# Performance work log

Hardware: AMD Instinct MI355X
Metric: run time of the kernel (lower is better)

## Reference

```python
import jax, jax.numpy as jnp
import numpy as np

HIDDEN = 1024
B, S = 8, 2048

def setup_inputs() -> dict:
    key = jax.random.key(0)
    k1, k2, k3, k4 = jax.random.split(key, 4)
    gain = 1.2
    # xavier_uniform bound for square [H,H] weight
    bound = gain * np.sqrt(6.0 / (HIDDEN + HIDDEN))
    return {
        "hidden_states": jax.random.normal(k1, (B, S, HIDDEN), dtype=jnp.float32),
        "Wq": jax.random.uniform(k2, (HIDDEN, HIDDEN), jnp.float32, -bound, bound),
        "bq": jnp.zeros((HIDDEN,), jnp.float32),
        "Wv": jax.random.uniform(k3, (HIDDEN, HIDDEN), jnp.float32, -bound, bound),
        "bv": jnp.zeros((HIDDEN,), jnp.float32),
        "anomaly_matrix": jax.random.uniform(k4, (HIDDEN, HIDDEN), jnp.float32, -2.0, 2.0),
    }

def reference(hidden_states, Wq, bq, Wv, bv, anomaly_matrix):
    # input magnitude rescaling
    input_norm = jnp.linalg.norm(hidden_states, axis=-1, keepdims=True)  # [B,S,1]
    scaled = hidden_states / (input_norm + 1e-9)
    # torch nn.Linear: x @ W.T + b
    q = jnp.einsum('bsh,oh->bso', scaled, Wq) + bq  # [B,S,H]
    v = jnp.einsum('bsh,oh->bso', scaled, Wv) + bv  # [B,S,H]
    # bilinear anomaly score: q @ A, then q @ (qA)^T
    tq = jnp.einsum('bsh,hk->bsk', q, anomaly_matrix)  # [B,S,H]
    scores = jnp.einsum('bsh,bth->bst', q, tq) / jnp.sqrt(jnp.float32(HIDDEN))  # [B,S,S]
    probs = jax.nn.softmax(scores, axis=-1)
    # dropout is identity in eval mode
    ctx = jnp.einsum('bst,bth->bsh', probs, v)  # [B,S,H]
    return ctx * input_norm
```

## Files before the change

kernel.cpp:

```cpp
#include <hip/hip_runtime.h>
#include <cstdint>
#include <cstddef>

#define H 1024
#define BB 8
#define SS 2048
#define MROWS (BB*SS)

typedef float  f32x4 __attribute__((ext_vector_type(4)));
typedef short  s16x8 __attribute__((ext_vector_type(8)));
typedef unsigned short u16x4 __attribute__((ext_vector_type(4)));
typedef unsigned short u16x8 __attribute__((ext_vector_type(8)));

__device__ __forceinline__ float b2f(unsigned short u) {
  union { unsigned int i; float f; } x; x.i = ((unsigned int)u) << 16; return x.f;
}
__device__ __forceinline__ unsigned short f2b(float f) {
  union { float f; unsigned int i; } x; x.f = f;
  unsigned int r = x.i + 0x7FFFu + ((x.i >> 16) & 1u);
  return (unsigned short)(r >> 16);
}

typedef __attribute__((address_space(1))) unsigned int guint;
typedef __attribute__((address_space(3))) unsigned int luint;
__device__ __forceinline__ void gld_lds16(const void* g, void* l) {
  __builtin_amdgcn_global_load_lds((guint*)g, (luint*)l, 16, 0, 0);
}

__global__ void norms_cast(const float* __restrict__ X, unsigned short* __restrict__ Xs,
                           float* __restrict__ norms) {
  const int row  = blockIdx.x * 4 + (threadIdx.x >> 6);
  const int lane = threadIdx.x & 63;
  const float4* xr = (const float4*)(X + (size_t)row * H);
  float4 d[4]; float s = 0.f;
#pragma unroll
  for (int j = 0; j < 4; ++j) {
    d[j] = xr[lane + j * 64];
    s += d[j].x*d[j].x + d[j].y*d[j].y + d[j].z*d[j].z + d[j].w*d[j].w;
  }
#pragma unroll
  for (int o = 32; o; o >>= 1) s += __shfl_xor(s, o);
  const float nrm = sqrtf(s);
  const float inv = 1.f / (nrm + 1e-9f);
  if (lane == 0) norms[row] = nrm;
  unsigned short* xo = Xs + (size_t)row * H;
#pragma unroll
  for (int j = 0; j < 4; ++j) {
    u16x4 o4;
    o4[0] = f2b(d[j].x * inv); o4[1] = f2b(d[j].y * inv);
    o4[2] = f2b(d[j].z * inv); o4[3] = f2b(d[j].w * inv);
    *(u16x4*)(xo + (size_t)(lane + j * 64) * 4) = o4;
  }
}

__global__ void cast_f32_bf16(const float* __restrict__ in, unsigned short* __restrict__ out) {
  const size_t i = ((size_t)blockIdx.x * 256 + threadIdx.x) * 4;
  float4 d = *(const float4*)(in + i);
  u16x4 o; o[0] = f2b(d.x); o[1] = f2b(d.y); o[2] = f2b(d.z); o[3] = f2b(d.w);
  *(u16x4*)(out + i) = o;
}

__global__ void transpose_cast_f32(const float* __restrict__ in, unsigned short* __restrict__ out) {
  __shared__ float t[32][33];
  const int c0 = blockIdx.x * 32, r0 = blockIdx.y * 32;
  const int tx = threadIdx.x, ty = threadIdx.y;
#pragma unroll
  for (int j = 0; j < 4; ++j)
    t[ty + j * 8][tx] = in[(size_t)(r0 + ty + j * 8) * H + c0 + tx];
  __syncthreads();
#pragma unroll
  for (int j = 0; j < 4; ++j)
    out[(size_t)(c0 + ty + j * 8) * H + r0 + tx] = f2b(t[tx][ty + j * 8]);
}

__global__ void transpose_bf16(const unsigned short* __restrict__ in, unsigned short* __restrict__ out) {
  __shared__ unsigned short t[32][33];
  const size_t zo = (size_t)blockIdx.z * SS * H;
  const int c0 = blockIdx.x * 32, r0 = blockIdx.y * 32;
  const int tx = threadIdx.x, ty = threadIdx.y;
#pragma unroll
  for (int j = 0; j < 4; ++j)
    t[ty + j * 8][tx] = in[zo + (size_t)(r0 + ty + j * 8) * H + c0 + tx];
  __syncthreads();
#pragma unroll
  for (int j = 0; j < 4; ++j)
    out[zo + (size_t)(c0 + ty + j * 8) * SS + r0 + tx] = t[tx][ty + j * 8];
}

template <int EPI, int TK>
__global__ __launch_bounds__(512, 2)
void gemm_nt(const unsigned short* __restrict__ A, int lda,
             const unsigned short* __restrict__ B0, int ldb, long sB,
             void* __restrict__ Cv, int ldc,
             const float* __restrict__ bias,
             const float* __restrict__ norms, const float* __restrict__ rs) {
  __shared__ __align__(16) unsigned short lds[4][2][256 * 32];
  const int tid = threadIdx.x, lane = tid & 63, w = tid >> 6;

  const int nx = gridDim.x;
  int bid = blockIdx.y * nx + blockIdx.x;
  bid = (bid & 7) * ((nx * (int)gridDim.y) >> 3) + (bid >> 3);
  const int bn = bid % nx, bm = bid / nx;

  const unsigned short* Ap = A  + (size_t)bm * 256 * lda;
  const unsigned short* Bp = B0 + (size_t)(bm >> 3) * sB + (size_t)bn * 256 * ldb;

  const int sr    = tid >> 2;
  const int gslot = (tid & 3) ^ ((sr >> 1) & 3);
  const unsigned short* As0 = Ap + (size_t)sr * lda + gslot * 8;
  const unsigned short* Bs0 = Bp + (size_t)sr * ldb + gslot * 8;

  auto STAGE = [&](int kt, int q) {
    const unsigned short* as = As0 + kt * 32;
    const unsigned short* bs = Bs0 + kt * 32;
    unsigned short* la = &lds[q][0][0] + tid * 8;
    unsigned short* lb = &lds[q][1][0] + tid * 8;
    gld_lds16(as,                       la);
    gld_lds16(as + (size_t)128 * lda,   la + 4096);
    gld_lds16(bs,                       lb);
    gld_lds16(bs + (size_t)128 * ldb,   lb + 4096);
  };

  const int wm = w >> 2, wn = w & 3;
  const int rA = lane & 15;
  const int ssw = ((lane >> 4) ^ ((rA >> 1) & 3)) * 8;
  f32x4 acc[8][4] = {};

  auto COMPUTE = [&](int t) {
    const unsigned short* pa = &lds[t & 3][0][0] + (size_t)(wm * 128 + rA) * 32 + ssw;
    const unsigned short* pb = &lds[t & 3][1][0] + (size_t)(wn * 64  + rA) * 32 + ssw;
    s16x8 af[8], bf[4];
#pragma unroll
    for (int i = 0; i < 8; ++i) af[i] = *(const s16x8*)(pa + i * 512);
#pragma unroll
    for (int j = 0; j < 4; ++j) bf[j] = *(const s16x8*)(pb + j * 512);
    __builtin_amdgcn_s_setprio(1);
#pragma unroll
    for (int i = 0; i < 8; ++i)
#pragma unroll
      for (int j = 0; j < 4; ++j)
        acc[i][j] = __builtin_amdgcn_mfma_f32_16x16x32_bf16(af[i], bf[j], acc[i][j], 0, 0, 0);
    __builtin_amdgcn_s_setprio(0);
  };

  STAGE(0, 0);
  STAGE(1, 1);
#pragma unroll 1
  for (int t = 0; t < TK - 2; ++t) {
    STAGE(t + 2, (t + 2) & 3);
    asm volatile("s_waitcnt vmcnt(8)" ::: "memory");
    __builtin_amdgcn_s_barrier();
    COMPUTE(t);
  }
  asm volatile("s_waitcnt vmcnt(4)" ::: "memory");
  __builtin_amdgcn_s_barrier();
  COMPUTE(TK - 2);
  asm volatile("s_waitcnt vmcnt(0)" ::: "memory");
  __builtin_amdgcn_s_barrier();
  COMPUTE(TK - 1);

  const int r0b = bm * 256 + wm * 128 + (lane >> 4) * 4;
  const int c0b = bn * 256 + wn * 64 + rA;
#pragma unroll
  for (int i = 0; i < 8; ++i) {
#pragma unroll
    for (int j = 0; j < 4; ++j) {
      const int cc = c0b + j * 16;
#pragma unroll
      for (int r = 0; r < 4; ++r) {
        const int rr = r0b + i * 16 + r;
        const size_t idx = (size_t)rr * ldc + cc;
        const float val = acc[i][j][r];
        if constexpr (EPI == 0) {
          ((unsigned short*)Cv)[idx] = f2b(val + bias[cc]);
        } else if constexpr (EPI == 1) {
          ((unsigned short*)Cv)[idx] = f2b(val);
        } else if constexpr (EPI == 2) {
          ((unsigned short*)Cv)[idx] = f2b(val * 0.03125f);
        } else {
          ((float*)Cv)[idx] = val * norms[rr] * rs[rr];
        }
      }
    }
  }
}

__global__ void softmax_rows(unsigned short* __restrict__ S, float* __restrict__ rs) {
  const int row = blockIdx.x;
  const int tid = threadIdx.x, lane = tid & 63, w = tid >> 6;
  unsigned short* sr = S + (size_t)row * SS;
  u16x8 raw = *(const u16x8*)(sr + tid * 8);
  float v[8]; float m = -1e30f;
#pragma unroll
  for (int j = 0; j < 8; ++j) { v[j] = b2f(raw[j]); m = fmaxf(m, v[j]); }
#pragma unroll
  for (int o = 32; o; o >>= 1) m = fmaxf(m, __shfl_xor(m, o));
  __shared__ float mx[4], sm[4];
  if (lane == 0) mx[w] = m;
  __syncthreads();
  m = fmaxf(fmaxf(mx[0], mx[1]), fmaxf(mx[2], mx[3]));
  float s = 0.f;
#pragma unroll
  for (int j = 0; j < 8; ++j) { v[j] = __expf(v[j] - m); s += v[j]; }
#pragma unroll
  for (int o = 32; o; o >>= 1) s += __shfl_xor(s, o);
  if (lane == 0) sm[w] = s;
  __syncthreads();
  s = sm[0] + sm[1] + sm[2] + sm[3];
  u16x8 ow;
#pragma unroll
  for (int j = 0; j < 8; ++j) ow[j] = f2b(v[j]);
  *(u16x8*)(sr + tid * 8) = ow;
  if (tid == 0) rs[row] = 1.0f / s;
}

extern "C" void kernel_launch(void* const* d_in, const int* in_sizes, int n_in,
                              void* d_out, int out_size, void* d_ws, size_t ws_size,
                              hipStream_t stream) {
  (void)in_sizes; (void)n_in; (void)out_size; (void)ws_size;
  const float* X  = (const float*)d_in[0];
  const float* Wq = (const float*)d_in[1];
  const float* bq = (const float*)d_in[2];
  const float* Wv = (const float*)d_in[3];
  const float* bv = (const float*)d_in[4];
  const float* Am = (const float*)d_in[5];

  char* ws = (char*)d_ws;
  size_t off = 0;
  auto alloc = [&](size_t bytes) { char* p = ws + off; off += (bytes + 255) & ~255ull; return p; };
  float* norms          = (float*)alloc((size_t)MROWS * 4);
  float* rs             = (float*)alloc((size_t)MROWS * 4);
  unsigned short* Wqb   = (unsigned short*)alloc((size_t)H * H * 2);
  unsigned short* Wvb   = (unsigned short*)alloc((size_t)H * H * 2);
  unsigned short* Atb   = (unsigned short*)alloc((size_t)H * H * 2);
  unsigned short* Qb    = (unsigned short*)alloc((size_t)MROWS * H * 2);
  unsigned short* TQb   = (unsigned short*)alloc((size_t)MROWS * H * 2);
  unsigned short* VTb   = (unsigned short*)alloc((size_t)MROWS * H * 2);
  unsigned short* Xs    = (unsigned short*)alloc((size_t)MROWS * H * 2);
  unsigned short* Vb    = (unsigned short*)alloc((size_t)MROWS * H * 2);
  unsigned short* Sc    = Xs;

  norms_cast<<<MROWS / 4, 256, 0, stream>>>(X, Xs, norms);
  cast_f32_bf16<<<H * H / 1024, 256, 0, stream>>>(Wq, Wqb);
  cast_f32_bf16<<<H * H / 1024, 256, 0, stream>>>(Wv, Wvb);
  transpose_cast_f32<<<dim3(H / 32, H / 32), dim3(32, 8), 0, stream>>>(Am, Atb);
  gemm_nt<0, 32><<<dim3(H / 256, MROWS / 256), 512, 0, stream>>>(Xs, H, Wqb, H, 0, Qb, H, bq, nullptr, nullptr);
  gemm_nt<0, 32><<<dim3(H / 256, MROWS / 256), 512, 0, stream>>>(Xs, H, Wvb, H, 0, Vb, H, bv, nullptr, nullptr);
  transpose_bf16<<<dim3(H / 32, SS / 32, BB), dim3(32, 8), 0, stream>>>(Vb, VTb);
  gemm_nt<1, 32><<<dim3(H / 256, MROWS / 256), 512, 0, stream>>>(Qb, H, Atb, H, 0, TQb, H, nullptr, nullptr, nullptr);
  gemm_nt<2, 32><<<dim3(SS / 256, MROWS / 256), 512, 0, stream>>>(Qb, H, TQb, H, (long)SS * H, Sc, SS, nullptr, nullptr, nullptr);
  softmax_rows<<<MROWS, 256, 0, stream>>>(Sc, rs);
  gemm_nt<3, 64><<<dim3(H / 256, MROWS / 256), 512, 0, stream>>>(Sc, SS, VTb, SS, (long)H * SS, d_out, H, nullptr, norms, rs);
}
```

Baseline: 408.0 us.

## Split GEMM k-tile into two half-phases interleaving LDS reads, prefetch, and MFMA

After: 416.6 us. 2.1% more time.

```diff
diff --git a/kernel.cpp b/kernel.cpp
--- a/kernel.cpp
+++ b/kernel.cpp
@@ -110,15 +110,17 @@
   const unsigned short* As0 = Ap + (size_t)sr * lda + gslot * 8;
   const unsigned short* Bs0 = Bp + (size_t)sr * ldb + gslot * 8;
 
-  auto STAGE = [&](int kt, int q) {
+  auto STAGE_A = [&](int kt) {
     const unsigned short* as = As0 + kt * 32;
+    unsigned short* la = &lds[kt & 3][0][0] + tid * 8;
+    gld_lds16(as,                     la);
+    gld_lds16(as + (size_t)128 * lda, la + 4096);
+  };
+  auto STAGE_B = [&](int kt) {
     const unsigned short* bs = Bs0 + kt * 32;
-    unsigned short* la = &lds[q][0][0] + tid * 8;
-    unsigned short* lb = &lds[q][1][0] + tid * 8;
-    gld_lds16(as,                       la);
-    gld_lds16(as + (size_t)128 * lda,   la + 4096);
-    gld_lds16(bs,                       lb);
-    gld_lds16(bs + (size_t)128 * ldb,   lb + 4096);
+    unsigned short* lb = &lds[kt & 3][1][0] + tid * 8;
+    gld_lds16(bs,                     lb);
+    gld_lds16(bs + (size_t)128 * ldb, lb + 4096);
   };
 
   const int wm = w >> 2, wn = w & 3;
@@ -126,38 +128,51 @@
   const int ssw = ((lane >> 4) ^ ((rA >> 1) & 3)) * 8;
   f32x4 acc[8][4] = {};
 
-  auto COMPUTE = [&](int t) {
+  auto TILE = [&](int t, int stk, int wmode) {
     const unsigned short* pa = &lds[t & 3][0][0] + (size_t)(wm * 128 + rA) * 32 + ssw;
     const unsigned short* pb = &lds[t & 3][1][0] + (size_t)(wn * 64  + rA) * 32 + ssw;
-    s16x8 af[8], bf[4];
-#pragma unroll
-    for (int i = 0; i < 8; ++i) af[i] = *(const s16x8*)(pa + i * 512);
+    s16x8 af[4], ag[4], bf[4];
+#pragma unroll
+    for (int i = 0; i < 4; ++i) af[i] = *(const s16x8*)(pa + i * 512);
 #pragma unroll
     for (int j = 0; j < 4; ++j) bf[j] = *(const s16x8*)(pb + j * 512);
+    if (stk >= 0) STAGE_A(stk);
+    __builtin_amdgcn_s_barrier();
+    asm volatile("s_waitcnt lgkmcnt(0)" ::: "memory");
     __builtin_amdgcn_s_setprio(1);
 #pragma unroll
-    for (int i = 0; i < 8; ++i)
+    for (int i = 0; i < 4; ++i)
 #pragma unroll
       for (int j = 0; j < 4; ++j)
         acc[i][j] = __builtin_amdgcn_mfma_f32_16x16x32_bf16(af[i], bf[j], acc[i][j], 0, 0, 0);
     __builtin_amdgcn_s_setprio(0);
+    __builtin_amdgcn_s_barrier();
+#pragma unroll
+    for (int i = 0; i < 4; ++i) ag[i] = *(const s16x8*)(pa + (4 + i) * 512);
+    if (stk >= 0) STAGE_B(stk);
+    if (wmode == 4)      asm volatile("s_waitcnt vmcnt(4)" ::: "memory");
+    else if (wmode == 0) asm volatile("s_waitcnt vmcnt(0)" ::: "memory");
+    __builtin_amdgcn_s_barrier();
+    asm volatile("s_waitcnt lgkmcnt(0)" ::: "memory");
+    __builtin_amdgcn_s_setprio(1);
+#pragma unroll
+    for (int i = 0; i < 4; ++i)
+#pragma unroll
+      for (int j = 0; j < 4; ++j)
+        acc[4 + i][j] = __builtin_amdgcn_mfma_f32_16x16x32_bf16(ag[i], bf[j], acc[4 + i][j], 0, 0, 0);
+    __builtin_amdgcn_s_setprio(0);
+    __builtin_amdgcn_s_barrier();
   };
 
-  STAGE(0, 0);
-  STAGE(1, 1);
-#pragma unroll 1
-  for (int t = 0; t < TK - 2; ++t) {
-    STAGE(t + 2, (t + 2) & 3);
-    asm volatile("s_waitcnt vmcnt(8)" ::: "memory");
-    __builtin_amdgcn_s_barrier();
-    COMPUTE(t);
-  }
+  STAGE_A(0); STAGE_B(0);
+  STAGE_A(1); STAGE_B(1);
   asm volatile("s_waitcnt vmcnt(4)" ::: "memory");
   __builtin_amdgcn_s_barrier();
-  COMPUTE(TK - 2);
-  asm volatile("s_waitcnt vmcnt(0)" ::: "memory");
-  __builtin_amdgcn_s_barrier();
-  COMPUTE(TK - 1);
+
+#pragma unroll 1
+  for (int t = 0; t < TK - 2; ++t) TILE(t, t + 2, 4);
+  TILE(TK - 2, -1, 0);
+  TILE(TK - 1, -1, -1);
 
   const int r0b = bm * 256 + wm * 128 + (lane >> 4) * 4;
   const int c0b = bn * 256 + wn * 64 + rA;
```

## Fuse exp into score GEMM epilogue and retile GEMMs to 128x128 with register prefetch

Applied to the files above, without the earlier changes.

Measured after the change: 437.6 us. +7.3%, slower.

```diff
diff --git a/kernel.cpp b/kernel.cpp
--- a/kernel.cpp
+++ b/kernel.cpp
@@ -88,13 +88,13 @@
 }
 
 template <int EPI, int TK>
-__global__ __launch_bounds__(512, 2)
+__global__ __launch_bounds__(256, 2)
 void gemm_nt(const unsigned short* __restrict__ A, int lda,
              const unsigned short* __restrict__ B0, int ldb, long sB,
              void* __restrict__ Cv, int ldc,
              const float* __restrict__ bias,
              const float* __restrict__ norms, const float* __restrict__ rs) {
-  __shared__ __align__(16) unsigned short lds[4][2][256 * 32];
+  __shared__ __align__(16) unsigned short lds[4][2][128 * 32];
   const int tid = threadIdx.x, lane = tid & 63, w = tid >> 6;
 
   const int nx = gridDim.x;
@@ -102,67 +102,73 @@
   bid = (bid & 7) * ((nx * (int)gridDim.y) >> 3) + (bid >> 3);
   const int bn = bid % nx, bm = bid / nx;
 
-  const unsigned short* Ap = A  + (size_t)bm * 256 * lda;
-  const unsigned short* Bp = B0 + (size_t)(bm >> 3) * sB + (size_t)bn * 256 * ldb;
+  const unsigned short* Ap = A  + (size_t)bm * 128 * lda;
+  const unsigned short* Bp = B0 + (size_t)(bm >> 4) * sB + (size_t)bn * 128 * ldb;
 
   const int sr    = tid >> 2;
   const int gslot = (tid & 3) ^ ((sr >> 1) & 3);
   const unsigned short* As0 = Ap + (size_t)sr * lda + gslot * 8;
   const unsigned short* Bs0 = Bp + (size_t)sr * ldb + gslot * 8;
 
-  auto STAGE = [&](int kt, int q) {
+  auto STAGE = [&](int kt) {
     const unsigned short* as = As0 + kt * 32;
     const unsigned short* bs = Bs0 + kt * 32;
-    unsigned short* la = &lds[q][0][0] + tid * 8;
-    unsigned short* lb = &lds[q][1][0] + tid * 8;
-    gld_lds16(as,                       la);
-    gld_lds16(as + (size_t)128 * lda,   la + 4096);
-    gld_lds16(bs,                       lb);
-    gld_lds16(bs + (size_t)128 * ldb,   lb + 4096);
-  };
-
-  const int wm = w >> 2, wn = w & 3;
+    unsigned short* la = &lds[kt & 3][0][0] + tid * 8;
+    unsigned short* lb = &lds[kt & 3][1][0] + tid * 8;
+    gld_lds16(as,                    la);
+    gld_lds16(as + (size_t)64 * lda, la + 2048);
+    gld_lds16(bs,                    lb);
+    gld_lds16(bs + (size_t)64 * ldb, lb + 2048);
+  };
+
+  const int wm = w >> 1, wn = w & 1;
   const int rA = lane & 15;
   const int ssw = ((lane >> 4) ^ ((rA >> 1) & 3)) * 8;
-  f32x4 acc[8][4] = {};
-
-  auto COMPUTE = [&](int t) {
-    const unsigned short* pa = &lds[t & 3][0][0] + (size_t)(wm * 128 + rA) * 32 + ssw;
-    const unsigned short* pb = &lds[t & 3][1][0] + (size_t)(wn * 64  + rA) * 32 + ssw;
-    s16x8 af[8], bf[4];
-#pragma unroll
-    for (int i = 0; i < 8; ++i) af[i] = *(const s16x8*)(pa + i * 512);
+
+  s16x8 afA[4], bfA[4], afB[4], bfB[4];
+  f32x4 acc[4][4] = {};
+
+  auto READ = [&](int kt, s16x8* af, s16x8* bf) {
+    const unsigned short* pa = &lds[kt & 3][0][0] + (size_t)(wm * 64 + rA) * 32 + ssw;
+    const unsigned short* pb = &lds[kt & 3][1][0] + (size_t)(wn * 64 + rA) * 32 + ssw;
+#pragma unroll
+    for (int i = 0; i < 4; ++i) af[i] = *(const s16x8*)(pa + i * 512);
 #pragma unroll
     for (int j = 0; j < 4; ++j) bf[j] = *(const s16x8*)(pb + j * 512);
+  };
+  auto MMA = [&](const s16x8* af, const s16x8* bf) {
     __builtin_amdgcn_s_setprio(1);
 #pragma unroll
-    for (int i = 0; i < 8; ++i)
+    for (int i = 0; i < 4; ++i)
 #pragma unroll
       for (int j = 0; j < 4; ++j)
         acc[i][j] = __builtin_amdgcn_mfma_f32_16x16x32_bf16(af[i], bf[j], acc[i][j], 0, 0, 0);
     __builtin_amdgcn_s_setprio(0);
   };
-
-  STAGE(0, 0);
-  STAGE(1, 1);
+  auto ITER = [&](int t, const s16x8* curA, const s16x8* curB, s16x8* nxtA, s16x8* nxtB) {
+    if (t <= TK - 3)      asm volatile("s_waitcnt vmcnt(4)" ::: "memory");
+    else if (t == TK - 2) asm volatile("s_waitcnt vmcnt(0)" ::: "memory");
+    __builtin_amdgcn_s_barrier();
+    if (t + 1 < TK) READ(t + 1, nxtA, nxtB);
+    if (t + 3 < TK) STAGE(t + 3);
+    MMA(curA, curB);
+  };
+
+  STAGE(0); STAGE(1); STAGE(2);
+  asm volatile("s_waitcnt vmcnt(8)" ::: "memory");
+  __builtin_amdgcn_s_barrier();
+  READ(0, afA, bfA);
+
 #pragma unroll 1
-  for (int t = 0; t < TK - 2; ++t) {
-    STAGE(t + 2, (t + 2) & 3);
-    asm volatile("s_waitcnt vmcnt(8)" ::: "memory");
-    __builtin_amdgcn_s_barrier();
-    COMPUTE(t);
-  }
-  asm volatile("s_waitcnt vmcnt(4)" ::: "memory");
-  __builtin_amdgcn_s_barrier();
-  COMPUTE(TK - 2);
-  asm volatile("s_waitcnt vmcnt(0)" ::: "memory");
-  __builtin_amdgcn_s_barrier();
-  COMPUTE(TK - 1);
-
-  const int r0b = bm * 256 + wm * 128 + (lane >> 4) * 4;
-  const int c0b = bn * 256 + wn * 64 + rA;
-#pragma unroll
-  for (int i = 0; i < 8; ++i) {
+  for (int t = 0; t < TK; t += 2) {
+    ITER(t,     afA, bfA, afB, bfB);
+    ITER(t + 1, afB, bfB, afA, bfA);
+  }
+
+  const int r0b = bm * 128 + wm * 64 + (lane >> 4) * 4;
+  const int c0b = bn * 128 + wn * 64 + rA;
+#pragma unroll
+  for (int i = 0; i < 4; ++i) {
 #pragma unroll
     for (int j = 0; j < 4; ++j) {
       const int cc = c0b + j * 16;
@@ -176,7 +182,7 @@
         } else if constexpr (EPI == 1) {
           ((unsigned short*)Cv)[idx] = f2b(val);
         } else if constexpr (EPI == 2) {
-          ((unsigned short*)Cv)[idx] = f2b(val * 0.03125f);
+          ((unsigned short*)Cv)[idx] = f2b(__expf(val * 0.03125f));
         } else {
           ((float*)Cv)[idx] = val * norms[rr] * rs[rr];
         }
@@ -185,33 +191,20 @@
   }
 }
 
-__global__ void softmax_rows(unsigned short* __restrict__ S, float* __restrict__ rs) {
+__global__ void rowsum(const unsigned short* __restrict__ S, float* __restrict__ rs) {
   const int row = blockIdx.x;
   const int tid = threadIdx.x, lane = tid & 63, w = tid >> 6;
-  unsigned short* sr = S + (size_t)row * SS;
+  const unsigned short* sr = S + (size_t)row * SS;
   u16x8 raw = *(const u16x8*)(sr + tid * 8);
-  float v[8]; float m = -1e30f;
-#pragma unroll
-  for (int j = 0; j < 8; ++j) { v[j] = b2f(raw[j]); m = fmaxf(m, v[j]); }
-#pragma unroll
-  for (int o = 32; o; o >>= 1) m = fmaxf(m, __shfl_xor(m, o));
-  __shared__ float mx[4], sm[4];
-  if (lane == 0) mx[w] = m;
-  __syncthreads();
-  m = fmaxf(fmaxf(mx[0], mx[1]), fmaxf(mx[2], mx[3]));
   float s = 0.f;
 #pragma unroll
-  for (int j = 0; j < 8; ++j) { v[j] = __expf(v[j] - m); s += v[j]; }
+  for (int j = 0; j < 8; ++j) s += b2f(raw[j]);
 #pragma unroll
   for (int o = 32; o; o >>= 1) s += __shfl_xor(s, o);
+  __shared__ float sm[4];
   if (lane == 0) sm[w] = s;
   __syncthreads();
-  s = sm[0] + sm[1] + sm[2] + sm[3];
-  u16x8 ow;
-#pragma unroll
-  for (int j = 0; j < 8; ++j) ow[j] = f2b(v[j]);
-  *(u16x8*)(sr + tid * 8) = ow;
-  if (tid == 0) rs[row] = 1.0f / s;
+  if (tid == 0) rs[row] = 1.0f / (sm[0] + sm[1] + sm[2] + sm[3]);
 }
 
 extern "C" void kernel_launch(void* const* d_in, const int* in_sizes, int n_in,
@@ -244,11 +237,11 @@
   cast_f32_bf16<<<H * H / 1024, 256, 0, stream>>>(Wq, Wqb);
   cast_f32_bf16<<<H * H / 1024, 256, 0, stream>>>(Wv, Wvb);
   transpose_cast_f32<<<dim3(H / 32, H / 32), dim3(32, 8), 0, stream>>>(Am, Atb);
-  gemm_nt<0, 32><<<dim3(H / 256, MROWS / 256), 512, 0, stream>>>(Xs, H, Wqb, H, 0, Qb, H, bq, nullptr, nullptr);
-  gemm_nt<0, 32><<<dim3(H / 256, MROWS / 256), 512, 0, stream>>>(Xs, H, Wvb, H, 0, Vb, H, bv, nullptr, nullptr);
+  gemm_nt<0, 32><<<dim3(H / 128, MROWS / 128), 256, 0, stream>>>(Xs, H, Wqb, H, 0, Qb, H, bq, nullptr, nullptr);
+  gemm_nt<0, 32><<<dim3(H / 128, MROWS / 128), 256, 0, stream>>>(Xs, H, Wvb, H, 0, Vb, H, bv, nullptr, nullptr);
   transpose_bf16<<<dim3(H / 32, SS / 32, BB), dim3(32, 8), 0, stream>>>(Vb, VTb);
-  gemm_nt<1, 32><<<dim3(H / 256, MROWS / 256), 512, 0, stream>>>(Qb, H, Atb, H, 0, TQb, H, nullptr, nullptr, nullptr);
-  gemm_nt<2, 32><<<dim3(SS / 256, MROWS / 256), 512, 0, stream>>>(Qb, H, TQb, H, (long)SS * H, Sc, SS, nullptr, nullptr, nullptr);
-  softmax_rows<<<MROWS, 256, 0, stream>>>(Sc, rs);
-  gemm_nt<3, 64><<<dim3(H / 256, MROWS / 256), 512, 0, stream>>>(Sc, SS, VTb, SS, (long)H * SS, d_out, H, nullptr, norms, rs);
-}
+  gemm_nt<1, 32><<<dim3(H / 128, MROWS / 128), 256, 0, stream>>>(Qb, H, Atb, H, 0, TQb, H, nullptr, nullptr, nullptr);
+  gemm_nt<2, 32><<<dim3(SS / 128, MROWS / 128), 256, 0, stream>>>(Qb, H, TQb, H, (long)SS * H, Sc, SS, nullptr, nullptr, nullptr);
+  rowsum<<<MROWS, 256, 0, stream>>>(Sc, rs);
+  gemm_nt<3, 64><<<dim3(H / 128, MROWS / 128), 256, 0, stream>>>(Sc, SS, VTb, SS, (long)H * SS, d_out, H, nullptr, norms, rs);
+}
```
